# Optimization experiments

Measured on AMD Instinct MI355X. Metric: run time of the kernel, lower is better.

## Reference

```python
import jax, jax.numpy as jnp
import numpy as np

B, S, H, W, DF, D, HID, ITERS = 8, 8, 64, 64, 64, 64, 128, 3
EPS = 1e-8


def build_grid(h, w):
    ranges = [np.linspace(-1.0, 1.0, num=h), np.linspace(-1.0, 1.0, num=w)]
    g = np.meshgrid(*ranges, sparse=False, indexing='xy')
    return jnp.asarray(np.stack(g, axis=-1), dtype=jnp.float32)  # [H, W, 2]


def ln(x, g, b):
    m = jnp.mean(x, axis=-1, keepdims=True)
    v = jnp.mean((x - m) ** 2, axis=-1, keepdims=True)
    return (x - m) * jax.lax.rsqrt(v + 1e-5) * g + b


def setup_inputs() -> dict:
    key = jax.random.key(0)
    ks = iter(jax.random.split(key, 64))
    def nrm(shape, s=0.02):
        return jax.random.normal(next(ks), shape, jnp.float32) * s
    inp = {}
    inp['inputs'] = jax.random.normal(next(ks), (B, H, W, DF), jnp.float32)
    # learned slot inits and learned per-slot position / scale factors
    inp['slots_p'] = jax.random.normal(next(ks), (1, S, D), jnp.float32)
    inp['s_pos_p'] = 2.0 * jax.random.uniform(next(ks), (1, S, 2), jnp.float32) - 1.0
    inp['s_scale_p'] = 0.1 + 0.01 * jax.random.normal(next(ks), (1, S, 2), jnp.float32)
    # soft position embedding Linear(2, D)
    inp['W_pos'] = nrm((2, D)); inp['b_pos'] = jnp.zeros((D,), jnp.float32)
    # q/k/v projections
    inp['Wq'] = nrm((D, D)); inp['bq'] = jnp.zeros((D,), jnp.float32)
    inp['Wk'] = nrm((DF, D)); inp['bk'] = jnp.zeros((D,), jnp.float32)
    inp['Wv'] = nrm((DF, D)); inp['bv'] = jnp.zeros((D,), jnp.float32)
    # layernorms
    inp['g_in'] = jnp.ones((DF,), jnp.float32); inp['b_in'] = jnp.zeros((DF,), jnp.float32)
    inp['g_slots'] = jnp.ones((D,), jnp.float32); inp['b_slots'] = jnp.zeros((D,), jnp.float32)
    inp['g_k'] = jnp.ones((D,), jnp.float32); inp['b_k'] = jnp.zeros((D,), jnp.float32)
    inp['g_v'] = jnp.ones((D,), jnp.float32); inp['b_v'] = jnp.zeros((D,), jnp.float32)
    # shared kv MLP fc1_kv / fc2_kv
    inp['W1'] = nrm((D, 2 * D)); inp['b1'] = jnp.zeros((2 * D,), jnp.float32)
    inp['W2'] = nrm((2 * D, D)); inp['b2'] = jnp.zeros((D,), jnp.float32)
    # GRUCell (torch layout transposed to [in, 3*D])
    inp['W_ih'] = nrm((D, 3 * D)); inp['b_ih'] = jnp.zeros((3 * D,), jnp.float32)
    inp['W_hh'] = nrm((D, 3 * D)); inp['b_hh'] = jnp.zeros((3 * D,), jnp.float32)
    # residual slot MLP
    inp['g_pre'] = jnp.ones((D,), jnp.float32); inp['b_pre'] = jnp.zeros((D,), jnp.float32)
    inp['Wf1'] = nrm((D, HID)); inp['bf1'] = jnp.zeros((HID,), jnp.float32)
    inp['Wf2'] = nrm((HID, D)); inp['bf2'] = jnp.zeros((D,), jnp.float32)
    return inp


def reference(inputs, slots_p, s_pos_p, s_scale_p, W_pos, b_pos, Wq, bq, Wk, bk, Wv, bv,
              g_in, b_in, g_slots, b_slots, g_k, b_k, g_v, b_v, W1, b1, W2, b2,
              W_ih, W_hh, b_ih, b_hh, g_pre, b_pre, Wf1, bf1, Wf2, bf2):
    grid = build_grid(H, W)                 # [H, W, 2]
    grid_flat = grid.reshape(-1, 2)          # [HW, 2]
    scale = D ** (-0.5)

    x = ln(inputs, g_in, b_in)
    k0 = x @ Wk + bk                         # [B, H, W, D]
    v0 = x @ Wv + bv

    slots = jnp.broadcast_to(slots_p, (B, S, D))
    s_pos = jnp.clip(jnp.broadcast_to(s_pos_p, (B, S, 2)), -1.0, 1.0)[:, :, None, None, :]
    s_scale = jnp.clip(jnp.broadcast_to(s_scale_p, (B, S, 2)), 1e-3, 2.0)[:, :, None, None, :]

    def proj_kv(base, sp, ss, g, b):
        gr = (grid[None, None] - sp) / (ss * 5.0)      # [B, S, H, W, 2]
        pe = gr @ W_pos + b_pos                        # [B, S, H, W, D]
        t = (base[:, None] + pe).reshape(B, S, H * W, D)
        t = ln(t, g, b)
        return jax.nn.relu(t @ W1 + b1) @ W2 + b2      # [B, S, HW, D]

    for i in range(ITERS + 1):
        slots_prev = slots
        q = ln(slots, g_slots, b_slots) @ Wq + bq       # [B, S, D]
        kk = proj_kv(k0, s_pos, s_scale, g_k, b_k)
        vv = proj_kv(v0, s_pos, s_scale, g_v, b_v)
        dots = jnp.einsum('bid,bijd->bij', q, kk) * scale
        attn_mask = jax.nn.softmax(dots, axis=1) + EPS  # softmax over slot axis
        attn = attn_mask / jnp.sum(attn_mask, axis=-1, keepdims=True)
        updates = jnp.einsum('bijd,bij->bid', vv, attn)
        if i < ITERS:
            xg = updates.reshape(-1, D) @ W_ih + b_ih
            hg = slots_prev.reshape(-1, D) @ W_hh + b_hh
            ir, iz, inn = jnp.split(xg, 3, axis=-1)
            hr, hz, hn = jnp.split(hg, 3, axis=-1)
            r = jax.nn.sigmoid(ir + hr)
            z = jax.nn.sigmoid(iz + hz)
            n = jnp.tanh(inn + r * hn)
            slots = ((1.0 - z) * n + z * slots_prev.reshape(-1, D)).reshape(B, S, D)
            slots = slots + (jax.nn.relu(ln(slots, g_pre, b_pre) @ Wf1 + bf1) @ Wf2 + bf2)
        else:
            slots = slots_prev
        # update per-slot position / scale from the attention mask
        sp = jnp.einsum('bij,jd->bid', attn_mask, grid_flat) / jnp.sum(attn_mask, axis=-1, keepdims=True)
        diff = grid_flat[None, None] - sp[:, :, None]   # [B, S, HW, 2]
        am = attn_mask + 1e-8
        ss = jnp.sqrt(jnp.einsum('bij,bijd->bid', am, diff ** 2) / jnp.sum(am, axis=-1, keepdims=True))
        s_pos = sp[:, :, None, None, :]
        s_scale = jnp.clip(ss, 1e-3, 2.0)[:, :, None, None, :]
    return slots, s_pos, s_scale, attn_mask
```

## Files before the change

kernel.cpp:

```cpp
#include <hip/hip_runtime.h>
#include <math.h>

typedef __bf16 bf16_t;
typedef __bf16 bfrag __attribute__((ext_vector_type(8)));
typedef float ffrag __attribute__((ext_vector_type(4)));

__device__ __forceinline__ float wave_sum(float v) {
#pragma unroll
  for (int m = 32; m >= 1; m >>= 1) v += __shfl_xor(v, m, 64);
  return v;
}
__device__ __forceinline__ float lin_(int i) { return -1.f + (2.f * (float)i) / 63.f; }
__device__ __forceinline__ float bflo(unsigned u) { return __uint_as_float(u << 16); }
__device__ __forceinline__ float bfhi(unsigned u) { return __uint_as_float(u & 0xFFFF0000u); }

__device__ __forceinline__ void pass_type(
    const bf16_t xs[][72], bf16_t t0s[][72],
    const bf16_t WTl[][72], const bf16_t W1l[][72],
    const float* __restrict__ bias, const float* wpxs, const float* wpys,
    const float* bpvs, float* __restrict__ statsG, bf16_t* __restrict__ P0G,
    int j0, int wv, int lq, int ln15) {
  ffrag C[4] = {{0,0,0,0},{0,0,0,0},{0,0,0,0},{0,0,0,0}};
#pragma unroll
  for (int ks = 0; ks < 2; ++ks) {
    bfrag a = *(const bfrag*)&xs[wv * 16 + ln15][ks * 32 + lq * 8];
#pragma unroll
    for (int nt = 0; nt < 4; ++nt) {
      bfrag bb = *(const bfrag*)&WTl[nt * 16 + ln15][ks * 32 + lq * 8];
      C[nt] = __builtin_amdgcn_mfma_f32_16x16x32_bf16(a, bb, C[nt], 0, 0, 0);
    }
  }
  float kv[4][4];
  float st[5][4];
#pragma unroll
  for (int i = 0; i < 5; ++i)
#pragma unroll
    for (int rg = 0; rg < 4; ++rg) st[i][rg] = 0.f;
#pragma unroll
  for (int nt = 0; nt < 4; ++nt) {
    int n = nt * 16 + ln15;
    float bn = bias[n], pxw = wpxs[n], pyw = wpys[n], bpw = bpvs[n];
#pragma unroll
    for (int rg = 0; rg < 4; ++rg) {
      float v = C[nt][rg] + bn;
      kv[nt][rg] = v;
      st[0][rg] += v; st[1][rg] += v * v; st[2][rg] += v * pxw;
      st[3][rg] += v * pyw; st[4][rg] += v * bpw;
    }
  }
#pragma unroll
  for (int i = 0; i < 5; ++i)
#pragma unroll
    for (int rg = 0; rg < 4; ++rg) {
      float v = st[i][rg];
      v += __shfl_xor(v, 1, 64); v += __shfl_xor(v, 2, 64);
      v += __shfl_xor(v, 4, 64); v += __shfl_xor(v, 8, 64);
      st[i][rg] = v;
    }
  if (ln15 == 0) {
#pragma unroll
    for (int rg = 0; rg < 4; ++rg) {
      int j = j0 + wv * 16 + lq * 4 + rg;
#pragma unroll
      for (int i = 0; i < 5; ++i) statsG[j * 5 + i] = st[i][rg];
    }
  }
#pragma unroll
  for (int nt = 0; nt < 4; ++nt)
#pragma unroll
    for (int rg = 0; rg < 4; ++rg)
      t0s[wv * 16 + lq * 4 + rg][nt * 16 + ln15] = (bf16_t)kv[nt][rg];
  ffrag D[8] = {{0,0,0,0},{0,0,0,0},{0,0,0,0},{0,0,0,0},
                {0,0,0,0},{0,0,0,0},{0,0,0,0},{0,0,0,0}};
#pragma unroll
  for (int ks = 0; ks < 2; ++ks) {
    bfrag a = *(const bfrag*)&t0s[wv * 16 + ln15][ks * 32 + lq * 8];
#pragma unroll
    for (int nt = 0; nt < 8; ++nt) {
      bfrag bb = *(const bfrag*)&W1l[nt * 16 + ln15][ks * 32 + lq * 8];
      D[nt] = __builtin_amdgcn_mfma_f32_16x16x32_bf16(a, bb, D[nt], 0, 0, 0);
    }
  }
#pragma unroll
  for (int nt = 0; nt < 8; ++nt)
#pragma unroll
    for (int rg = 0; rg < 4; ++rg)
      P0G[(size_t)(j0 + wv * 16 + lq * 4 + rg) * 128 + nt * 16 + ln15] =
          (bf16_t)D[nt][rg];
}

__global__ __launch_bounds__(256) void k_pre(
    const float* __restrict__ inp, const float* __restrict__ g_in,
    const float* __restrict__ b_in, const float* __restrict__ bk,
    const float* __restrict__ bv, const float* __restrict__ Wk,
    const float* __restrict__ Wv, const float* __restrict__ W1,
    const float* __restrict__ g_k, const float* __restrict__ g_v,
    const float* __restrict__ W_pos, const float* __restrict__ b_pos,
    bf16_t* __restrict__ P0k, bf16_t* __restrict__ P0v,
    float* __restrict__ statsK, float* __restrict__ statsV,
    const float* __restrict__ slots_p, const float* __restrict__ g_slots,
    const float* __restrict__ b_slots, const float* __restrict__ Wq,
    const float* __restrict__ bq, const float* __restrict__ W2,
    const float* __restrict__ b2, float* __restrict__ w2qg,
    float* __restrict__ b2qg,
    const float* __restrict__ b_k, const float* __restrict__ b_v,
    const float* __restrict__ b1, const float* __restrict__ s_pos_p,
    const float* __restrict__ s_scale_p,
    float4* __restrict__ nckA, float* __restrict__ nckB,
    float4* __restrict__ ncvA, float* __restrict__ ncvB,
    float* __restrict__ possum, float* __restrict__ sposS,
    float* __restrict__ sscaleS, float* __restrict__ slotsS) {
  __shared__ bf16_t xs[64][72];
  __shared__ bf16_t t0s[64][72];
  __shared__ bf16_t WkTl[64][72];
  __shared__ bf16_t WvTl[64][72];
  __shared__ bf16_t W1kl[128][72];
  __shared__ bf16_t W1vl[128][72];
  __shared__ float wpxs[64], wpys[64], bpvs[64];
  const int tid = threadIdx.x;
  const int j0 = blockIdx.x * 64;
  for (int i = tid; i < 4096; i += 256) {
    int n = i & 63, d = i >> 6;
    WkTl[n][d] = (bf16_t)Wk[i];
    WvTl[n][d] = (bf16_t)Wv[i];
  }
  for (int i = tid; i < 8192; i += 256) {
    int n = i & 127, c = i >> 7;
    float w = W1[i];
    W1kl[n][c] = (bf16_t)(g_k[c] * w);
    W1vl[n][c] = (bf16_t)(g_v[c] * w);
  }
  if (tid < 64) { wpxs[tid] = W_pos[tid]; wpys[tid] = W_pos[64 + tid]; bpvs[tid] = b_pos[tid]; }
  {
    const int px = tid >> 2, cg = tid & 3;
    const float* rowp = inp + (size_t)(j0 + px) * 64 + cg * 16;
    float v[16];
    *(float4*)&v[0]  = ((const float4*)rowp)[0];
    *(float4*)&v[4]  = ((const float4*)rowp)[1];
    *(float4*)&v[8]  = ((const float4*)rowp)[2];
    *(float4*)&v[12] = ((const float4*)rowp)[3];
    float s = 0.f, s2 = 0.f;
#pragma unroll
    for (int i = 0; i < 16; ++i) { s += v[i]; s2 += v[i] * v[i]; }
    s += __shfl_xor(s, 1, 64); s += __shfl_xor(s, 2, 64);
    s2 += __shfl_xor(s2, 1, 64); s2 += __shfl_xor(s2, 2, 64);
    float m = s * 0.015625f;
    float r = rsqrtf(s2 * 0.015625f - m * m + 1e-5f);
    float g[16], bb[16];
    *(float4*)&g[0]  = ((const float4*)(g_in + cg * 16))[0];
    *(float4*)&g[4]  = ((const float4*)(g_in + cg * 16))[1];
    *(float4*)&g[8]  = ((const float4*)(g_in + cg * 16))[2];
    *(float4*)&g[12] = ((const float4*)(g_in + cg * 16))[3];
    *(float4*)&bb[0]  = ((const float4*)(b_in + cg * 16))[0];
    *(float4*)&bb[4]  = ((const float4*)(b_in + cg * 16))[1];
    *(float4*)&bb[8]  = ((const float4*)(b_in + cg * 16))[2];
    *(float4*)&bb[12] = ((const float4*)(b_in + cg * 16))[3];
#pragma unroll
    for (int e = 0; e < 8; ++e) {
      float x0 = (v[2 * e] - m) * r * g[2 * e] + bb[2 * e];
      float x1 = (v[2 * e + 1] - m) * r * g[2 * e + 1] + bb[2 * e + 1];
      union { unsigned u; bf16_t h[2]; } cv;
      cv.h[0] = (bf16_t)x0; cv.h[1] = (bf16_t)x1;
      *(unsigned*)&xs[px][cg * 16 + 2 * e] = cv.u;
    }
  }
  __syncthreads();
  const int wv = tid >> 6, lane = tid & 63, lq = lane >> 4, ln15 = lane & 15;
  pass_type(xs, t0s, WkTl, W1kl, bk, wpxs, wpys, bpvs, statsK, P0k, j0, wv, lq, ln15);
  __syncthreads();
  pass_type(xs, t0s, WvTl, W1vl, bv, wpxs, wpys, bpvs, statsV, P0v, j0, wv, lq, ln15);
  if (blockIdx.x < 64 && tid < 64) {
    int bs = blockIdx.x, d = tid;
    float v = slots_p[(bs & 7) * 64 + d];
    float m = wave_sum(v) * 0.015625f;
    float c = v - m;
    float var = wave_sum(c * c) * 0.015625f;
    float xn = c * rsqrtf(var + 1e-5f) * g_slots[d] + b_slots[d];
    float q = bq[d];
    for (int cc = 0; cc < 64; ++cc) q = fmaf(__shfl(xn, cc, 64), Wq[cc * 64 + d], q);
    float w0 = 0.f, w1 = 0.f;
    for (int cc = 0; cc < 64; ++cc) {
      float qc = __shfl(q, cc, 64);
      w0 = fmaf(W2[d * 64 + cc], qc, w0);
      w1 = fmaf(W2[(64 + d) * 64 + cc], qc, w1);
    }
    w2qg[bs * 128 + d] = w0;
    w2qg[bs * 128 + 64 + d] = w1;
    float p = wave_sum(b2[d] * q);
    if (d == 0) b2qg[bs] = p;
  }
  if (blockIdx.x == 508 && tid < 128) {
    int n = tid;
    float wx = 0, wy = 0, wb = 0, u = 0, sk = 0;
    for (int c = 0; c < 64; ++c) {
      float w = W1[c * 128 + n];
      float wf = g_k[c] * w;
      float px = W_pos[c], py = W_pos[64 + c], bp = b_pos[c];
      wx += px * wf; wy += py * wf; wb += bp * wf; sk += wf; u += b_k[c] * w;
    }
    nckA[n] = make_float4(wx, wy, wb, u + b1[n]); nckB[n] = sk;
  }
  if (blockIdx.x == 509 && tid < 128) {
    int n = tid;
    float wx = 0, wy = 0, wb = 0, u = 0, sv = 0;
    for (int c = 0; c < 64; ++c) {
      float w = W1[c * 128 + n];
      float wf = g_v[c] * w;
      float px = W_pos[c], py = W_pos[64 + c], bp = b_pos[c];
      wx += px * wf; wy += py * wf; wb += bp * wf; sv += wf; u += b_v[c] * w;
    }
    ncvA[n] = make_float4(wx, wy, wb, u + b1[n]); ncvB[n] = sv;
  }
  if (blockIdx.x == 510) {
    if (tid < 64) {
      float px = W_pos[tid], py = W_pos[64 + tid], bp = b_pos[tid];
      float s9[9] = {px, py, bp, px * px, py * py, bp * bp, px * py, px * bp, py * bp};
#pragma unroll
      for (int i = 0; i < 9; ++i) {
        float v = wave_sum(s9[i]);
        if (tid == 0) possum[i] = v;
      }
    }
    if (tid < 128) {
      sposS[tid] = fminf(fmaxf(s_pos_p[tid & 15], -1.f), 1.f);
      sscaleS[tid] = fminf(fmaxf(s_scale_p[tid & 15], 0.001f), 2.f);
    }
    for (int i = tid; i < 4096; i += 256) slotsS[i] = slots_p[i & 511];
  }
}

template <int LAST>
__global__ __launch_bounds__(256, 4) void k_iter(
    const bf16_t* __restrict__ P0kg, const bf16_t* __restrict__ P0vg,
    const float* __restrict__ statsK, const float* __restrict__ statsV,
    const float4* __restrict__ nckA, const float* __restrict__ nckB,
    const float4* __restrict__ ncvA, const float* __restrict__ ncvB,
    const float* __restrict__ possum, const float* __restrict__ w2qg,
    const float* __restrict__ b2qg, const float* __restrict__ sposS,
    const float* __restrict__ sscaleS, float* __restrict__ momP,
    float* __restrict__ HsumP, float* __restrict__ outAttn) {
  __shared__ unsigned P0vl[32 * 65];
  __shared__ float ncqT[128 * 16];
  __shared__ float4 scalV[32][9];
  __shared__ float attnS[32][10];
  __shared__ float momAcc[8][5];
  const int tid = threadIdx.x;
  const int tile = blockIdx.x, b = blockIdx.y;
  const int jg0 = b * 4096 + tile * 32;
  const int px = tid >> 3, sp = tid & 7;
  uint4 pk0 = ((const uint4*)P0kg)[(size_t)(jg0 + px) * 16 + sp * 2 + 0];
  uint4 pk1 = ((const uint4*)P0kg)[(size_t)(jg0 + px) * 16 + sp * 2 + 1];
  float skA[5], svA[5];
#pragma unroll
  for (int i = 0; i < 5; ++i) {
    skA[i] = statsK[(size_t)(jg0 + px) * 5 + i];
    if (!LAST) svA[i] = statsV[(size_t)(jg0 + px) * 5 + i];
  }
  if (!LAST) {
#pragma unroll
    for (int r = 0; r < 2; ++r) {
      int idx = tid + 256 * r;
      int row = idx >> 4, seg = idx & 15;
      uint4 w = ((const uint4*)P0vg)[(size_t)(jg0 + row) * 16 + seg];
      unsigned* d2 = &P0vl[row * 65 + seg * 4];
      d2[0] = w.x; d2[1] = w.y; d2[2] = w.z; d2[3] = w.w;
    }
  }
  {
    int n = tid & 127, g = tid >> 7, r4 = ((n >> 4) & 3) * 4;
    float* row = &ncqT[n * 16];
    if (g == 0) {
      float4 A = nckA[n];
      row[(0 + r4) & 15] = A.x; row[(1 + r4) & 15] = A.y;
      row[(2 + r4) & 15] = A.z; row[(3 + r4) & 15] = A.w;
#pragma unroll
      for (int s = 0; s < 4; ++s) row[(4 + s + r4) & 15] = w2qg[(b * 8 + s) * 128 + n];
    } else {
#pragma unroll
      for (int s = 4; s < 8; ++s) row[(4 + s + r4) & 15] = w2qg[(b * 8 + s) * 128 + n];
      row[(12 + r4) & 15] = nckB[n];
    }
  }
  if (tid < 40) momAcc[tid / 5][tid % 5] = 0.f;
  __syncthreads();

  const int jimg = tile * 32 + px;
  const float gx = lin_(jimg & 63), gy = lin_(jimg >> 6);
  const float Swx = possum[0], Swy = possum[1], Sbp = possum[2];
  const float Swx2 = possum[3], Swy2 = possum[4], Sbp2 = possum[5];
  const float Swxy = possum[6], Swxb = possum[7], Swyb = possum[8];
  float c1a[8], c2a[8], rKa[8], mrKa[8];
#pragma unroll
  for (int s = 0; s < 8; ++s) {
    int bs = b * 8 + s;
    float spx = sposS[bs * 2], spy = sposS[bs * 2 + 1];
    float rxx = 1.f / (sscaleS[bs * 2] * 5.f);
    float ryy = 1.f / (sscaleS[bs * 2 + 1] * 5.f);
    float c1 = (gx - spx) * rxx, c2 = (gy - spy) * ryy;
    float quad = c1 * c1 * Swx2 + c2 * c2 * Swy2 + Sbp2 +
                 2.f * (c1 * c2 * Swxy + c1 * Swxb + c2 * Swyb);
    float mK = (skA[0] + c1 * Swx + c2 * Swy + Sbp) * 0.015625f;
    float e2K = (skA[1] + 2.f * (c1 * skA[2] + c2 * skA[3] + skA[4]) + quad) * 0.015625f;
    float rK = rsqrtf(e2K - mK * mK + 1e-5f);
    c1a[s] = c1; c2a[s] = c2; rKa[s] = rK; mrKa[s] = mK * rK;
    if (!LAST && s == sp) {
      float mV = (svA[0] + c1 * Swx + c2 * Swy + Sbp) * 0.015625f;
      float e2V = (svA[1] + 2.f * (c1 * svA[2] + c2 * svA[3] + svA[4]) + quad) * 0.015625f;
      float rV = rsqrtf(e2V - mV * mV + 1e-5f);
      scalV[px][s] = make_float4(c1, c2, rV, mV * rV);
    }
  }
  const unsigned uu[8] = {pk0.x, pk0.y, pk0.z, pk0.w, pk1.x, pk1.y, pk1.z, pk1.w};
  const int r4 = (sp & 3) * 4;
  float d8[8] = {0, 0, 0, 0, 0, 0, 0, 0};
#pragma unroll
  for (int i = 0; i < 8; ++i) {
    int n0 = 16 * sp + 2 * i;
    const float* R0 = &ncqT[n0 * 16];
    const float* R1 = R0 + 16;
    float4 A0 = *(const float4*)&R0[r4];
    float4 q0a = *(const float4*)&R0[(r4 + 4) & 15];
    float4 q0b = *(const float4*)&R0[(r4 + 8) & 15];
    float ws0 = R0[(r4 + 12) & 15];
    float4 A1 = *(const float4*)&R1[r4];
    float4 q1a = *(const float4*)&R1[(r4 + 4) & 15];
    float4 q1b = *(const float4*)&R1[(r4 + 8) & 15];
    float ws1 = R1[(r4 + 12) & 15];
    float qq0[8] = {q0a.x, q0a.y, q0a.z, q0a.w, q0b.x, q0b.y, q0b.z, q0b.w};
    float qq1[8] = {q1a.x, q1a.y, q1a.z, q1a.w, q1b.x, q1b.y, q1b.z, q1b.w};
    float p0 = bflo(uu[i]), p1 = bfhi(uu[i]);
    float bm0 = p0 + A0.z, bm1 = p1 + A1.z;
#pragma unroll
    for (int s = 0; s < 8; ++s) {
      float z0 = bm0 + c1a[s] * A0.x + c2a[s] * A0.y;
      float h0 = fmaxf(fmaf(rKa[s], z0, fmaf(-mrKa[s], ws0, A0.w)), 0.f);
      d8[s] = fmaf(h0, qq0[s], d8[s]);
      float z1 = bm1 + c1a[s] * A1.x + c2a[s] * A1.y;
      float h1 = fmaxf(fmaf(rKa[s], z1, fmaf(-mrKa[s], ws1, A1.w)), 0.f);
      d8[s] = fmaf(h1, qq1[s], d8[s]);
    }
  }
#pragma unroll
  for (int s = 0; s < 8; ++s) {
    float v = d8[s];
    v += __shfl_xor(v, 1, 64);
    v += __shfl_xor(v, 2, 64);
    v += __shfl_xor(v, 4, 64);
    d8[s] = (v + b2qg[b * 8 + s]) * 0.125f;
  }
  float mx = d8[0];
#pragma unroll
  for (int s = 1; s < 8; ++s) mx = fmaxf(mx, d8[s]);
  float tt = 0.f;
  float e8[8];
#pragma unroll
  for (int s = 0; s < 8; ++s) { e8[s] = expf(d8[s] - mx); tt += e8[s]; }
  float inv = 1.f / tt;
#pragma unroll
  for (int s = 0; s < 8; ++s) e8[s] = e8[s] * inv + 1e-8f;
  attnS[px][sp] = e8[sp];
  if (LAST) outAttn[(size_t)(b * 8 + sp) * 4096 + jimg] = e8[sp];
  {
    float w = e8[sp];
    float mm[5] = {w, w * gx, w * gy, w * gx * gx, w * gy * gy};
#pragma unroll
    for (int i = 0; i < 5; ++i) {
      float v = mm[i];
      v += __shfl_xor(v, 8, 64); v += __shfl_xor(v, 16, 64);
      v += __shfl_xor(v, 32, 64);
      mm[i] = v;
    }
    if ((tid & 63) < 8) {
#pragma unroll
      for (int i = 0; i < 5; ++i) atomicAdd(&momAcc[sp][i], mm[i]);
    }
  }
  __syncthreads();
  if (tid < 40)
    momP[((size_t)(b * 8 + tid / 5) * 128 + tile) * 5 + tid % 5] =
        momAcc[tid / 5][tid % 5];

  if (!LAST) {
    const int w = tid >> 6, l = tid & 63;
    const int s0 = 2 * w, s1 = 2 * w + 1;
    float4 cv0 = ncvA[2 * l], cv1 = ncvA[2 * l + 1];
    float wv0 = ncvB[2 * l], wv1 = ncvB[2 * l + 1];
    float h00 = 0.f, h01 = 0.f, h10 = 0.f, h11 = 0.f;
#pragma unroll 4
    for (int j = 0; j < 32; ++j) {
      unsigned u = P0vl[j * 65 + l];
      float pv0 = bflo(u), pv1 = bfhi(u);
      float bm0 = pv0 + cv0.z, bm1 = pv1 + cv1.z;
      float4 sa = scalV[j][s0]; float aw = attnS[j][s0];
      float z0 = bm0 + sa.x * cv0.x + sa.y * cv0.y;
      h00 = fmaf(aw, fmaxf(fmaf(sa.z, z0, fmaf(-sa.w, wv0, cv0.w)), 0.f), h00);
      float z1 = bm1 + sa.x * cv1.x + sa.y * cv1.y;
      h01 = fmaf(aw, fmaxf(fmaf(sa.z, z1, fmaf(-sa.w, wv1, cv1.w)), 0.f), h01);
      float4 sb = scalV[j][s1]; float ab = attnS[j][s1];
      float z2 = bm0 + sb.x * cv0.x + sb.y * cv0.y;
      h10 = fmaf(ab, fmaxf(fmaf(sb.z, z2, fmaf(-sb.w, wv0, cv0.w)), 0.f), h10);
      float z3 = bm1 + sb.x * cv1.x + sb.y * cv1.y;
      h11 = fmaf(ab, fmaxf(fmaf(sb.z, z3, fmaf(-sb.w, wv1, cv1.w)), 0.f), h11);
    }
    *(float2*)&HsumP[((size_t)(b * 8 + s0) * 128 + tile) * 128 + 2 * l] =
        make_float2(h00, h01);
    *(float2*)&HsumP[((size_t)(b * 8 + s1) * 128 + tile) * 128 + 2 * l] =
        make_float2(h10, h11);
  }
}

__global__ __launch_bounds__(192) void k_fin(
    const float* __restrict__ momP, const float* __restrict__ HsumP,
    const float* __restrict__ W2, const float* __restrict__ b2,
    const float* __restrict__ W_ih, const float* __restrict__ b_ih,
    const float* __restrict__ W_hh, const float* __restrict__ b_hh,
    const float* __restrict__ g_pre, const float* __restrict__ b_pre,
    const float* __restrict__ Wf1, const float* __restrict__ bf1,
    const float* __restrict__ Wf2, const float* __restrict__ bf2,
    const float* __restrict__ g_slots, const float* __restrict__ b_slots,
    const float* __restrict__ Wq, const float* __restrict__ bq,
    float* __restrict__ slotsS, float* __restrict__ sposS, float* __restrict__ sscaleS,
    float* __restrict__ w2qg, float* __restrict__ b2qg,
    float* __restrict__ outSlots, float* __restrict__ outSpos,
    float* __restrict__ outSscale, int last) {
  const int bs = blockIdx.x;
  const int t = threadIdx.x;
  __shared__ float hsum_s[128], upd[64], sprev[64], xg[192], hg[192];
  __shared__ float snew[64], xpre[64], hf[128], sfin[64], xn[64], qsh[64];
  __shared__ float mom_s[5];
  if (t < 64) {
    const float* mp = momP + ((size_t)bs * 128 + t) * 5;
    float m0 = mp[0] + mp[320], m1 = mp[1] + mp[321], m2 = mp[2] + mp[322];
    float m3 = mp[3] + mp[323], m4 = mp[4] + mp[324];
    m0 = wave_sum(m0); m1 = wave_sum(m1); m2 = wave_sum(m2);
    m3 = wave_sum(m3); m4 = wave_sum(m4);
    if (t == 0) { mom_s[0] = m0; mom_s[1] = m1; mom_s[2] = m2; mom_s[3] = m3; mom_s[4] = m4; }
    if (!last) sprev[t] = slotsS[bs * 64 + t];
  }
  if (!last && t >= 64) {
    int n = t - 64;
    const float* hp = HsumP + (size_t)bs * 16384 + n;
    float a = 0.f;
#pragma unroll 8
    for (int tile = 0; tile < 128; ++tile) a += hp[tile * 128];
    hsum_s[n] = a;
  }
  __syncthreads();
  const float M0 = mom_s[0];
  const float M1x = mom_s[1], M1y = mom_s[2];
  const float M2x = mom_s[3], M2y = mom_s[4];
  const float invM0 = 1.f / M0;
  const float spx = M1x * invM0, spy = M1y * invM0;
  const float M0a = M0 + 4096.f * 1e-8f;
  const float G2 = 1408.6772487f * 1e-8f;
  const float vx = (M2x + G2 - 2.f * spx * M1x + spx * spx * M0a) / M0a;
  const float vy = (M2y + G2 - 2.f * spy * M1y + spy * spy * M0a) / M0a;
  float ssx = sqrtf(fmaxf(vx, 0.f)), ssy = sqrtf(fmaxf(vy, 0.f));
  ssx = fminf(fmaxf(ssx, 0.001f), 2.f);
  ssy = fminf(fmaxf(ssy, 0.001f), 2.f);
  if (t == 0) {
    sposS[bs * 2 + 0] = spx; sposS[bs * 2 + 1] = spy;
    sscaleS[bs * 2 + 0] = ssx; sscaleS[bs * 2 + 1] = ssy;
    if (last) {
      outSpos[bs * 2 + 0] = spx; outSpos[bs * 2 + 1] = spy;
      outSscale[bs * 2 + 0] = ssx; outSscale[bs * 2 + 1] = ssy;
    }
  }
  if (last) {
    if (t < 64) outSlots[bs * 64 + t] = slotsS[bs * 64 + t];
    return;
  }
  if (t < 64) {
    float a = 0.f;
#pragma unroll
    for (int k = 0; k < 128; ++k) a += hsum_s[k] * W2[k * 64 + t];
    upd[t] = a * invM0 + b2[t];
  }
  __syncthreads();
  {
    float a = b_ih[t], h = b_hh[t];
#pragma unroll
    for (int d = 0; d < 64; ++d) {
      a += upd[d] * W_ih[d * 192 + t];
      h += sprev[d] * W_hh[d * 192 + t];
    }
    xg[t] = a; hg[t] = h;
  }
  __syncthreads();
  if (t < 64) {
    float r = 1.f / (1.f + expf(-(xg[t] + hg[t])));
    float z = 1.f / (1.f + expf(-(xg[64 + t] + hg[64 + t])));
    float n = tanhf(xg[128 + t] + r * hg[128 + t]);
    snew[t] = (1.f - z) * n + z * sprev[t];
  }
  __syncthreads();
  if (t < 64) {
    float v = snew[t];
    float m = wave_sum(v) * 0.015625f;
    float c = v - m;
    float var = wave_sum(c * c) * 0.015625f;
    xpre[t] = c * rsqrtf(var + 1e-5f) * g_pre[t] + b_pre[t];
  }
  __syncthreads();
  if (t < 128) {
    float a = bf1[t];
#pragma unroll
    for (int d = 0; d < 64; ++d) a += xpre[d] * Wf1[d * 128 + t];
    hf[t] = fmaxf(a, 0.f);
  }
  __syncthreads();
  if (t < 64) {
    float a = bf2[t];
#pragma unroll
    for (int k = 0; k < 128; ++k) a += hf[k] * Wf2[k * 64 + t];
    float nv = snew[t] + a;
    slotsS[bs * 64 + t] = nv;
    sfin[t] = nv;
  }
  __syncthreads();
  if (t < 64) {
    float v = sfin[t];
    float m = wave_sum(v) * 0.015625f;
    float c = v - m;
    float var = wave_sum(c * c) * 0.015625f;
    xn[t] = c * rsqrtf(var + 1e-5f) * g_slots[t] + b_slots[t];
  }
  __syncthreads();
  if (t < 64) {
    float a = bq[t];
#pragma unroll
    for (int d = 0; d < 64; ++d) a += xn[d] * Wq[d * 64 + t];
    qsh[t] = a;
  }
  __syncthreads();
  if (t < 128) {
    float a = 0.f;
#pragma unroll
    for (int d = 0; d < 64; ++d) a += W2[t * 64 + d] * qsh[d];
    w2qg[bs * 128 + t] = a;
  }
  if (t < 64) {
    float p = wave_sum(b2[t] * qsh[t]);
    if (t == 0) b2qg[bs] = p;
  }
}

extern "C" void kernel_launch(void* const* d_in, const int* in_sizes, int n_in,
                              void* d_out, int out_size, void* d_ws, size_t ws_size,
                              hipStream_t stream) {
  (void)in_sizes; (void)n_in; (void)out_size; (void)ws_size;
  const float* const* in = (const float* const*)d_in;
  float* ws = (float*)d_ws;
  bf16_t* P0k   = (bf16_t*)(ws + 0);
  bf16_t* P0v   = (bf16_t*)(ws + 2097152);
  float* statsK = ws + 4194304;
  float* statsV = ws + 4358144;
  float* w2qg   = ws + 4521984;
  float* b2qg   = ws + 4530176;
  float* slotsS = ws + 4530240;
  float* sposS  = ws + 4534336;
  float* sscaleS= ws + 4534464;
  float4* nckA  = (float4*)(ws + 4555392);
  float* nckB   = ws + 4555904;
  float4* ncvA  = (float4*)(ws + 4556032);
  float* ncvB   = ws + 4556544;
  float* possum = ws + 4556672;
  float* HsumP  = ws + 4560896;
  float* momP   = ws + 5609472;

  float* out = (float*)d_out;
  float* outSlots  = out;
  float* outSpos   = out + 4096;
  float* outSscale = out + 4224;
  float* outAttn   = out + 4352;

  k_pre<<<512, 256, 0, stream>>>(
      in[0], in[12], in[13], in[9], in[11], in[8], in[10], in[20], in[16], in[18],
      in[4], in[5], P0k, P0v, statsK, statsV,
      in[1], in[14], in[15], in[6], in[7], in[22], in[23], w2qg, b2qg,
      in[17], in[19], in[21], in[2], in[3],
      nckA, nckB, ncvA, ncvB, possum, sposS, sscaleS, slotsS);
  for (int i = 0; i < 4; ++i) {
    int last = (i == 3) ? 1 : 0;
    if (!last) {
      k_iter<0><<<dim3(128, 8), 256, 0, stream>>>(
          P0k, P0v, statsK, statsV, nckA, nckB, ncvA, ncvB, possum,
          w2qg, b2qg, sposS, sscaleS, momP, HsumP, outAttn);
    } else {
      k_iter<1><<<dim3(128, 8), 256, 0, stream>>>(
          P0k, P0v, statsK, statsV, nckA, nckB, ncvA, ncvB, possum,
          w2qg, b2qg, sposS, sscaleS, momP, HsumP, outAttn);
    }
    k_fin<<<64, 192, 0, stream>>>(momP, HsumP, in[22], in[23], in[24], in[25],
                                  in[26], in[27], in[28], in[29], in[30], in[31],
                                  in[32], in[33], in[14], in[15], in[6], in[7],
                                  slotsS, sposS, sscaleS, w2qg, b2qg,
                                  outSlots, outSpos, outSscale, last);
  }
}
```

Before: 269.1 us.

## Interleave K/V stats into one buffer and remap blocks for XCD locality

```diff
diff --git a/kernel.cpp b/kernel.cpp
--- a/kernel.cpp
+++ b/kernel.cpp
@@ -62,7 +62,7 @@
     for (int rg = 0; rg < 4; ++rg) {
       int j = j0 + wv * 16 + lq * 4 + rg;
 #pragma unroll
-      for (int i = 0; i < 5; ++i) statsG[j * 5 + i] = st[i][rg];
+      for (int i = 0; i < 5; ++i) statsG[(size_t)j * 10 + i] = st[i][rg];
     }
   }
 #pragma unroll
@@ -97,7 +97,7 @@
     const float* __restrict__ g_k, const float* __restrict__ g_v,
     const float* __restrict__ W_pos, const float* __restrict__ b_pos,
     bf16_t* __restrict__ P0k, bf16_t* __restrict__ P0v,
-    float* __restrict__ statsK, float* __restrict__ statsV,
+    float* __restrict__ statsC,
     const float* __restrict__ slots_p, const float* __restrict__ g_slots,
     const float* __restrict__ b_slots, const float* __restrict__ Wq,
     const float* __restrict__ bq, const float* __restrict__ W2,
@@ -166,9 +166,9 @@
   }
   __syncthreads();
   const int wv = tid >> 6, lane = tid & 63, lq = lane >> 4, ln15 = lane & 15;
-  pass_type(xs, t0s, WkTl, W1kl, bk, wpxs, wpys, bpvs, statsK, P0k, j0, wv, lq, ln15);
-  __syncthreads();
-  pass_type(xs, t0s, WvTl, W1vl, bv, wpxs, wpys, bpvs, statsV, P0v, j0, wv, lq, ln15);
+  pass_type(xs, t0s, WkTl, W1kl, bk, wpxs, wpys, bpvs, statsC, P0k, j0, wv, lq, ln15);
+  __syncthreads();
+  pass_type(xs, t0s, WvTl, W1vl, bv, wpxs, wpys, bpvs, statsC + 5, P0v, j0, wv, lq, ln15);
   if (blockIdx.x < 64 && tid < 64) {
     int bs = blockIdx.x, d = tid;
     float v = slots_p[(bs & 7) * 64 + d];
@@ -232,7 +232,7 @@
 template <int LAST>
 __global__ __launch_bounds__(256, 4) void k_iter(
     const bf16_t* __restrict__ P0kg, const bf16_t* __restrict__ P0vg,
-    const float* __restrict__ statsK, const float* __restrict__ statsV,
+    const float* __restrict__ statsC,
     const float4* __restrict__ nckA, const float* __restrict__ nckB,
     const float4* __restrict__ ncvA, const float* __restrict__ ncvB,
     const float* __restrict__ possum, const float* __restrict__ w2qg,
@@ -245,16 +245,28 @@
   __shared__ float attnS[32][10];
   __shared__ float momAcc[8][5];
   const int tid = threadIdx.x;
-  const int tile = blockIdx.x, b = blockIdx.y;
+  const int L = blockIdx.x + 128 * blockIdx.y;
+  const int xcd = L & 7, cc_ = (L >> 3) & 15, b = L >> 7;
+  const int tile = 2 * (xcd + 8 * (cc_ >> 1)) + (cc_ & 1);
   const int jg0 = b * 4096 + tile * 32;
   const int px = tid >> 3, sp = tid & 7;
   uint4 pk0 = ((const uint4*)P0kg)[(size_t)(jg0 + px) * 16 + sp * 2 + 0];
   uint4 pk1 = ((const uint4*)P0kg)[(size_t)(jg0 + px) * 16 + sp * 2 + 1];
   float skA[5], svA[5];
-#pragma unroll
-  for (int i = 0; i < 5; ++i) {
-    skA[i] = statsK[(size_t)(jg0 + px) * 5 + i];
-    if (!LAST) svA[i] = statsV[(size_t)(jg0 + px) * 5 + i];
+  {
+    const int lb = (tid & 63) & ~7;
+    float sv0 = statsC[(size_t)(jg0 + px) * 10 + sp];
+    float sv1 = 0.f;
+    if (!LAST && sp < 2) sv1 = statsC[(size_t)(jg0 + px) * 10 + 8 + sp];
+#pragma unroll
+    for (int i = 0; i < 5; ++i) skA[i] = __shfl(sv0, lb + i, 64);
+    if (!LAST) {
+      svA[0] = __shfl(sv0, lb + 5, 64);
+      svA[1] = __shfl(sv0, lb + 6, 64);
+      svA[2] = __shfl(sv0, lb + 7, 64);
+      svA[3] = __shfl(sv1, lb + 0, 64);
+      svA[4] = __shfl(sv1, lb + 1, 64);
+    }
   }
   if (!LAST) {
 #pragma unroll
@@ -553,8 +565,7 @@
   float* ws = (float*)d_ws;
   bf16_t* P0k   = (bf16_t*)(ws + 0);
   bf16_t* P0v   = (bf16_t*)(ws + 2097152);
-  float* statsK = ws + 4194304;
-  float* statsV = ws + 4358144;
+  float* statsC = ws + 4194304;
   float* w2qg   = ws + 4521984;
   float* b2qg   = ws + 4530176;
   float* slotsS = ws + 4530240;
@@ -576,7 +587,7 @@
 
   k_pre<<<512, 256, 0, stream>>>(
       in[0], in[12], in[13], in[9], in[11], in[8], in[10], in[20], in[16], in[18],
-      in[4], in[5], P0k, P0v, statsK, statsV,
+      in[4], in[5], P0k, P0v, statsC,
       in[1], in[14], in[15], in[6], in[7], in[22], in[23], w2qg, b2qg,
       in[17], in[19], in[21], in[2], in[3],
       nckA, nckB, ncvA, ncvB, possum, sposS, sscaleS, slotsS);
@@ -584,11 +595,11 @@
     int last = (i == 3) ? 1 : 0;
     if (!last) {
       k_iter<0><<<dim3(128, 8), 256, 0, stream>>>(
-          P0k, P0v, statsK, statsV, nckA, nckB, ncvA, ncvB, possum,
+          P0k, P0v, statsC, nckA, nckB, ncvA, ncvB, possum,
           w2qg, b2qg, sposS, sscaleS, momP, HsumP, outAttn);
     } else {
       k_iter<1><<<dim3(128, 8), 256, 0, stream>>>(
-          P0k, P0v, statsK, statsV, nckA, nckB, ncvA, ncvB, possum,
+          P0k, P0v, statsC, nckA, nckB, ncvA, ncvB, possum,
           w2qg, b2qg, sposS, sscaleS, momP, HsumP, outAttn);
     }
     k_fin<<<64, 192, 0, stream>>>(momP, HsumP, in[22], in[23], in[24], in[25],
```

Measured after the change: 268.0 us. Within noise of the previous version (-0.4%).
